# Optimization experiments

Measured on AMD Instinct MI355X. Metric: run time of the kernel, lower is better.

## Reference

```python
import jax, jax.numpy as jnp
import numpy as np

EPS = 1e-5  # haiku LayerNorm default


def _layernorm_last(x, scale, offset):
    m = jnp.mean(x, axis=-1, keepdims=True)
    v = jnp.var(x, axis=-1, keepdims=True)
    return (x - m) * jax.lax.rsqrt(v + EPS) * scale + offset


def setup_inputs() -> dict:
    key = jax.random.key(0)
    ks = jax.random.split(key, 6)
    N, C = 512, 128
    return {
        "act": jax.random.normal(ks[0], (N, N, C), dtype=jnp.float32),
        "mask": jnp.ones((N, N), dtype=jnp.float32),
        "ln_scale": jnp.ones((C,), dtype=jnp.float32),
        "ln_offset": jnp.zeros((C,), dtype=jnp.float32),
        "w_proj": jax.random.normal(ks[1], (C, 2 * C), dtype=jnp.float32) * 0.02,
        "w_gate": jax.random.normal(ks[2], (C, 2 * C), dtype=jnp.float32) * 0.02,
        "cn_scale": jnp.ones((C,), dtype=jnp.float32),
        "cn_offset": jnp.zeros((C,), dtype=jnp.float32),
        "w_out": jax.random.normal(ks[3], (C, C), dtype=jnp.float32) * 0.02,
        "b_out": jnp.zeros((C,), dtype=jnp.float32),
        "w_gate_out": jax.random.normal(ks[4], (C, C), dtype=jnp.float32) * 0.02,
        "b_gate_out": jnp.ones((C,), dtype=jnp.float32),  # bias_init=1.0
    }


def reference(act, mask, ln_scale, ln_offset, w_proj, w_gate,
              cn_scale, cn_offset, w_out, b_out, w_gate_out, b_gate_out):
    C = act.shape[-1]
    # left_norm_input (LayerNorm over channel axis)
    x = _layernorm_last(act, ln_scale, ln_offset)  # [N,N,C]
    input_act = x
    # gated linear unit: projection * sigmoid(gate), no biases (GLU kernel path)
    proj = jnp.einsum('ijc,cd->ijd', x, w_proj) * jax.nn.sigmoid(
        jnp.einsum('ijc,cd->ijd', x, w_gate))  # [N,N,2C]
    proj = jnp.transpose(proj, (2, 0, 1)) * mask[None]  # [2C,N,N]
    # split even/odd channels: reshape(C,2,N,N) -> a=proj[:,0], b=proj[:,1]
    proj = proj.reshape(C, 2, *proj.shape[1:])
    a, b = proj[:, 0], proj[:, 1]  # each [C,N,N]
    # triangle einsum ('ikc,jkc->ijc' -> 'cik,cjk->cij')
    act2 = jnp.einsum('cik,cjk->cij', a, b)  # [C,N,N]
    # center_norm: LayerNorm over channel axis (axis=0), params on axis 0
    m = jnp.mean(act2, axis=0, keepdims=True)
    v = jnp.var(act2, axis=0, keepdims=True)
    act2 = (act2 - m) * jax.lax.rsqrt(v + EPS) * cn_scale[:, None, None] + cn_offset[:, None, None]
    out = jnp.transpose(act2, (1, 2, 0))  # [N,N,C]
    out = jnp.einsum('ijc,cd->ijd', out, w_out) + b_out
    gate_out = jax.nn.sigmoid(jnp.einsum('ijc,cd->ijd', input_act, w_gate_out) + b_gate_out)
    return out * gate_out
```

## Files before the change

kernel.cpp:

```cpp
#include <hip/hip_runtime.h>
#include <stdint.h>

#define NDIM 512
#define CDIM 128
#define MDIM (NDIM*NDIM)

typedef unsigned short u16;
typedef __bf16 bf16v8 __attribute__((ext_vector_type(8)));
typedef float f32x4 __attribute__((ext_vector_type(4)));
typedef short s16x4 __attribute__((ext_vector_type(4)));

__device__ __forceinline__ u16 f2bf(float f){
  union { float f; uint32_t u; } v; v.f = f;
  uint32_t u = v.u;
  u += 0x7fffu + ((u >> 16) & 1u);
  return (u16)(u >> 16);
}
__device__ __forceinline__ float sigm(float x){ return 1.0f/(1.0f + __expf(-x)); }
__device__ __forceinline__ f32x4 mfma_bf16(bf16v8 a, bf16v8 b, f32x4 c){
  return __builtin_amdgcn_mfma_f32_16x16x32_bf16(a, b, c, 0, 0, 0);
}

__global__ void k0_prep(const float* __restrict__ wp, const float* __restrict__ wg,
                        const float* __restrict__ wgo, const float* __restrict__ wo,
                        u16* __restrict__ wt){
  const int d = blockIdx.x, k = threadIdx.x;
  float v;
  if (d < 256)      v = wp[k*256 + d];
  else if (d < 512) v = wg[k*256 + (d-256)];
  else if (d < 640) v = wgo[k*128 + (d-512)];
  else              v = wo[k*128 + (d-640)];
  wt[d*CDIM + k] = f2bf(v);
}

__global__ __launch_bounds__(256) void k1_ln_proj(
    const float* __restrict__ act, const float* __restrict__ mask,
    const float* __restrict__ lns, const float* __restrict__ lno,
    const float* __restrict__ bgo, const u16* __restrict__ wt,
    u16* __restrict__ AB, float* __restrict__ gate)
{
  __shared__ __align__(16) u16 xs[64][136];
  __shared__ __align__(16) u16 pgs[256][72];
  __shared__ float msk[64];
  const int t = threadIdx.x;
  const int m0 = blockIdx.x * 64;

  {
    const int r = t >> 2, q = t & 3;
    const float4* rp = (const float4*)(act + (size_t)(m0 + r)*CDIM + q*32);
    float4 v[8];
    #pragma unroll
    for (int i = 0; i < 8; ++i) v[i] = rp[i];
    float s = 0.f, s2 = 0.f;
    #pragma unroll
    for (int i = 0; i < 8; ++i){
      s  += v[i].x + v[i].y + v[i].z + v[i].w;
      s2 += v[i].x*v[i].x + v[i].y*v[i].y + v[i].z*v[i].z + v[i].w*v[i].w;
    }
    s += __shfl_xor(s, 1);  s2 += __shfl_xor(s2, 1);
    s += __shfl_xor(s, 2);  s2 += __shfl_xor(s2, 2);
    const float mean = s * (1.f/128.f);
    const float rstd = rsqrtf(s2 * (1.f/128.f) - mean*mean + 1e-5f);
    const float4* lsp = (const float4*)(lns + q*32);
    const float4* lop = (const float4*)(lno + q*32);
    #pragma unroll
    for (int i = 0; i < 8; ++i){
      const float4 sc = lsp[i], of = lop[i];
      s16x4 pk;
      pk.x = (short)f2bf((v[i].x - mean)*rstd*sc.x + of.x);
      pk.y = (short)f2bf((v[i].y - mean)*rstd*sc.y + of.y);
      pk.z = (short)f2bf((v[i].z - mean)*rstd*sc.z + of.z);
      pk.w = (short)f2bf((v[i].w - mean)*rstd*sc.w + of.w);
      *(s16x4*)&xs[r][q*32 + i*4] = pk;
    }
    if (t < 64) msk[t] = mask[m0 + t];
  }
  __syncthreads();

  const int w = t >> 6, L = t & 63, ln16 = L & 15, quad = L >> 4;
  bf16v8 af[4][4];
  #pragma unroll
  for (int rs = 0; rs < 4; ++rs)
    #pragma unroll
    for (int kk = 0; kk < 4; ++kk)
      af[rs][kk] = *(const bf16v8*)&xs[rs*16 + ln16][kk*32 + quad*8];

  const f32x4 zero4 = {0.f,0.f,0.f,0.f};
  #pragma unroll
  for (int pp = 0; pp < 4; ++pp){
    const int p = w*4 + pp;
    const u16* wpr = wt + (size_t)(16*p + ln16)*CDIM + quad*8;
    const u16* wgr = wpr + (size_t)256*CDIM;
    bf16v8 bp[4], bg[4];
    #pragma unroll
    for (int kk = 0; kk < 4; ++kk){
      bp[kk] = *(const bf16v8*)(wpr + kk*32);
      bg[kk] = *(const bf16v8*)(wgr + kk*32);
    }
    f32x4 aP[4] = {zero4, zero4, zero4, zero4};
    f32x4 aG[4] = {zero4, zero4, zero4, zero4};
    #pragma unroll
    for (int kk = 0; kk < 4; ++kk)
      #pragma unroll
      for (int rs = 0; rs < 4; ++rs){
        aP[rs] = mfma_bf16(af[rs][kk], bp[kk], aP[rs]);
        aG[rs] = mfma_bf16(af[rs][kk], bg[kk], aG[rs]);
      }
    #pragma unroll
    for (int rs = 0; rs < 4; ++rs)
      #pragma unroll
      for (int reg = 0; reg < 4; ++reg){
        const int ml = rs*16 + quad*4 + reg;
        const float pg = aP[rs][reg] * sigm(aG[rs][reg]) * msk[ml];
        pgs[16*p + ln16][ml] = f2bf(pg);
      }
  }
  #pragma unroll
  for (int u = 0; u < 2; ++u){
    const int e0 = 32*w + 16*u;
    const u16* wr = wt + (size_t)(512 + e0 + ln16)*CDIM + quad*8;
    bf16v8 bb[4];
    #pragma unroll
    for (int kk = 0; kk < 4; ++kk) bb[kk] = *(const bf16v8*)(wr + kk*32);
    f32x4 ag[4] = {zero4, zero4, zero4, zero4};
    #pragma unroll
    for (int kk = 0; kk < 4; ++kk)
      #pragma unroll
      for (int rs = 0; rs < 4; ++rs)
        ag[rs] = mfma_bf16(af[rs][kk], bb[kk], ag[rs]);
    const int e = e0 + ln16;
    const float bias = bgo[e];
    #pragma unroll
    for (int rs = 0; rs < 4; ++rs)
      #pragma unroll
      for (int reg = 0; reg < 4; ++reg){
        const int ml = rs*16 + quad*4 + reg;
        gate[(size_t)(m0 + ml)*CDIM + e] = sigm(ag[rs][reg] + bias);
      }
  }
  __syncthreads();

  #pragma unroll
  for (int p4 = 0; p4 < 4; ++p4){
    const int d = p4*64 + (t >> 2), q = t & 3;
    u16* dst = AB + (size_t)d*MDIM + m0 + q*16;
    const u16* src = &pgs[d][q*16];
    *(bf16v8*)dst       = *(const bf16v8*)src;
    *(bf16v8*)(dst + 8) = *(const bf16v8*)(src + 8);
  }
}

__global__ __launch_bounds__(256) void k2_tri(const u16* __restrict__ AB,
                                              u16* __restrict__ act2)
{
  __shared__ __align__(16) u16 As[128][72];
  __shared__ __align__(16) u16 Bs[128][72];
  const int t = threadIdx.x, bid = blockIdx.x;
  const int c  = bid >> 4;
  const int i0 = ((bid >> 2) & 3) * 128;
  const int j0 = (bid & 3) * 128;
  const u16* Ag = AB + (size_t)(2*c)*MDIM;
  const u16* Bg = AB + (size_t)(2*c + 1)*MDIM;

  const int w = t >> 6, L = t & 63, ln16 = L & 15, quad = L >> 4;
  const int iw = (w & 1)*64, jw = (w >> 1)*64;
  const int r = t >> 1, h = t & 1;

  const f32x4 zero4 = {0.f,0.f,0.f,0.f};
  f32x4 acc[4][4];
  #pragma unroll
  for (int x = 0; x < 4; ++x)
    #pragma unroll
    for (int y = 0; y < 4; ++y) acc[x][y] = zero4;

  for (int k0 = 0; k0 < NDIM; k0 += 64){
    const u16* ga = Ag + (size_t)(i0 + r)*NDIM + k0 + h*32;
    const u16* gb = Bg + (size_t)(j0 + r)*NDIM + k0 + h*32;
    bf16v8 sa[4], sb[4];
    #pragma unroll
    for (int x = 0; x < 4; ++x){
      sa[x] = *(const bf16v8*)(ga + x*8);
      sb[x] = *(const bf16v8*)(gb + x*8);
    }
    __syncthreads();
    #pragma unroll
    for (int x = 0; x < 4; ++x){
      *(bf16v8*)&As[r][h*32 + x*8] = sa[x];
      *(bf16v8*)&Bs[r][h*32 + x*8] = sb[x];
    }
    __syncthreads();
    #pragma unroll
    for (int kk = 0; kk < 2; ++kk){
      bf16v8 ar[4], br[4];
      #pragma unroll
      for (int x = 0; x < 4; ++x) ar[x] = *(const bf16v8*)&As[iw + x*16 + ln16][kk*32 + quad*8];
      #pragma unroll
      for (int y = 0; y < 4; ++y) br[y] = *(const bf16v8*)&Bs[jw + y*16 + ln16][kk*32 + quad*8];
      #pragma unroll
      for (int x = 0; x < 4; ++x)
        #pragma unroll
        for (int y = 0; y < 4; ++y)
          acc[x][y] = mfma_bf16(ar[x], br[y], acc[x][y]);
    }
  }

  u16* op = act2 + (size_t)c*MDIM;
  #pragma unroll
  for (int x = 0; x < 4; ++x)
    #pragma unroll
    for (int y = 0; y < 4; ++y)
      #pragma unroll
      for (int reg = 0; reg < 4; ++reg){
        const int il = iw + x*16 + quad*4 + reg;
        const int jl = jw + y*16 + ln16;
        op[(size_t)(i0 + il)*NDIM + j0 + jl] = f2bf(acc[x][y][reg]);
      }
}

__global__ __launch_bounds__(256) void k3_out(
    const u16* __restrict__ act2, const u16* __restrict__ wt2,
    const float* __restrict__ cns, const float* __restrict__ cno,
    const float* __restrict__ bo, float* __restrict__ out)
{
  __shared__ __align__(16) float vs[128][65];
  __shared__ __align__(16) u16 xs2[64][136];
  __shared__ float csh[128], coh[128];
  const int t = threadIdx.x;
  const int i  = blockIdx.x >> 3;
  const int j0 = (blockIdx.x & 7)*64;
  if (t < 128){ csh[t] = cns[t]; coh[t] = cno[t]; }

  {
    const int cc = t >> 1, h = t & 1;
    const u16* g = act2 + (size_t)cc*MDIM + (size_t)i*NDIM + j0 + h*32;
    #pragma unroll
    for (int x = 0; x < 4; ++x){
      bf16v8 uv = *(const bf16v8*)(g + x*8);
      #pragma unroll
      for (int e = 0; e < 8; ++e) vs[cc][h*32 + x*8 + e] = (float)uv[e];
    }
  }
  __syncthreads();
  {
    const int jj = t >> 2, q = t & 3;
    float s = 0.f, s2 = 0.f;
    #pragma unroll
    for (int ci = 0; ci < 32; ++ci){
      const float v = vs[4*ci + q][jj];
      s += v; s2 += v*v;
    }
    s += __shfl_xor(s,1); s2 += __shfl_xor(s2,1);
    s += __shfl_xor(s,2); s2 += __shfl_xor(s2,2);
    const float mean = s*(1.f/128.f);
    const float rstd = rsqrtf(s2*(1.f/128.f) - mean*mean + 1e-5f);
    #pragma unroll
    for (int ci = 0; ci < 32; ++ci){
      const int cc = 4*ci + q;
      xs2[jj][cc] = f2bf((vs[cc][jj] - mean)*rstd*csh[cc] + coh[cc]);
    }
  }
  __syncthreads();

  const int w = t >> 6, L = t & 63, ln16 = L & 15, quad = L >> 4;
  bf16v8 af[4];
  #pragma unroll
  for (int kk = 0; kk < 4; ++kk)
    af[kk] = *(const bf16v8*)&xs2[w*16 + ln16][kk*32 + quad*8];
  const f32x4 zero4 = {0.f,0.f,0.f,0.f};
  #pragma unroll
  for (int n = 0; n < 8; ++n){
    const u16* wr = wt2 + (size_t)(n*16 + ln16)*CDIM + quad*8;
    bf16v8 bb[4];
    #pragma unroll
    for (int kk = 0; kk < 4; ++kk) bb[kk] = *(const bf16v8*)(wr + kk*32);
    f32x4 ac = zero4;
    #pragma unroll
    for (int kk = 0; kk < 4; ++kk) ac = mfma_bf16(af[kk], bb[kk], ac);
    const int e = n*16 + ln16;
    const float bias = bo[e];
    #pragma unroll
    for (int reg = 0; reg < 4; ++reg){
      const int jl = w*16 + quad*4 + reg;
      const size_t idx = ((size_t)i*NDIM + j0 + jl)*(size_t)CDIM + e;
      out[idx] = (ac[reg] + bias) * out[idx];
    }
  }
}

extern "C" void kernel_launch(void* const* d_in, const int* in_sizes, int n_in,
                              void* d_out, int out_size, void* d_ws, size_t ws_size,
                              hipStream_t stream)
{
  const float* act = (const float*)d_in[0];
  const float* msk = (const float*)d_in[1];
  const float* lns = (const float*)d_in[2];
  const float* lno = (const float*)d_in[3];
  const float* wp  = (const float*)d_in[4];
  const float* wg  = (const float*)d_in[5];
  const float* cns = (const float*)d_in[6];
  const float* cno = (const float*)d_in[7];
  const float* wo  = (const float*)d_in[8];
  const float* bo  = (const float*)d_in[9];
  const float* wgo = (const float*)d_in[10];
  const float* bgo = (const float*)d_in[11];
  float* out = (float*)d_out;

  u16* AB   = (u16*)d_ws;
  u16* ACT2 = AB + (size_t)256*MDIM;
  u16* WT   = ACT2 + (size_t)128*MDIM;

  k0_prep   <<<dim3(768),  dim3(128), 0, stream>>>(wp, wg, wgo, wo, WT);
  k1_ln_proj<<<dim3(4096), dim3(256), 0, stream>>>(act, msk, lns, lno, bgo, WT, AB, out);
  k2_tri    <<<dim3(2048), dim3(256), 0, stream>>>(AB, ACT2);
  k3_out    <<<dim3(4096), dim3(256), 0, stream>>>(ACT2, WT + 640*CDIM, cns, cno, bo, out);
}
```

Baseline: 546.3 us.

## Recompute output gate in final kernel instead of round-tripping through output buffer

Moves the sigmoid output-gate projection out of the first kernel into the final kernel. The final kernel now re-reads the fp32 input, redoes the LayerNorm and computes the gate GEMM next to the output GEMM. This removes a 128 MB fp32 write and a 128 MB read of the gate through the output buffer, at the cost of re-reading the 128 MB fp32 input. It also stores the staging tiles as bf16 instead of fp32 to cut shared memory, and adds a minimum-blocks occupancy hint to both kernels.

```diff
diff --git a/kernel.cpp b/kernel.cpp
--- a/kernel.cpp
+++ b/kernel.cpp
@@ -9,12 +9,17 @@
 typedef __bf16 bf16v8 __attribute__((ext_vector_type(8)));
 typedef float f32x4 __attribute__((ext_vector_type(4)));
 typedef short s16x4 __attribute__((ext_vector_type(4)));
+
+union V16 { bf16v8 v; s16x4 h[2]; };
 
 __device__ __forceinline__ u16 f2bf(float f){
   union { float f; uint32_t u; } v; v.f = f;
   uint32_t u = v.u;
   u += 0x7fffu + ((u >> 16) & 1u);
   return (u16)(u >> 16);
+}
+__device__ __forceinline__ float bf2f(u16 x){
+  union { uint32_t u; float f; } v; v.u = ((uint32_t)x) << 16; return v.f;
 }
 __device__ __forceinline__ float sigm(float x){ return 1.0f/(1.0f + __expf(-x)); }
 __device__ __forceinline__ f32x4 mfma_bf16(bf16v8 a, bf16v8 b, f32x4 c){
@@ -33,14 +38,13 @@
   wt[d*CDIM + k] = f2bf(v);
 }
 
-__global__ __launch_bounds__(256) void k1_ln_proj(
+__global__ __launch_bounds__(256, 3) void k1_ln_proj(
     const float* __restrict__ act, const float* __restrict__ mask,
     const float* __restrict__ lns, const float* __restrict__ lno,
-    const float* __restrict__ bgo, const u16* __restrict__ wt,
-    u16* __restrict__ AB, float* __restrict__ gate)
+    const u16* __restrict__ wt, u16* __restrict__ AB)
 {
   __shared__ __align__(16) u16 xs[64][136];
-  __shared__ __align__(16) u16 pgs[256][72];
+  __shared__ __align__(8)  u16 pgs[256][68];
   __shared__ float msk[64];
   const int t = threadIdx.x;
   const int m0 = blockIdx.x * 64;
@@ -107,36 +111,16 @@
         aG[rs] = mfma_bf16(af[rs][kk], bg[kk], aG[rs]);
       }
     #pragma unroll
-    for (int rs = 0; rs < 4; ++rs)
+    for (int rs = 0; rs < 4; ++rs){
+      s16x4 pk;
       #pragma unroll
       for (int reg = 0; reg < 4; ++reg){
         const int ml = rs*16 + quad*4 + reg;
         const float pg = aP[rs][reg] * sigm(aG[rs][reg]) * msk[ml];
-        pgs[16*p + ln16][ml] = f2bf(pg);
+        ((short*)&pk)[reg] = (short)f2bf(pg);
       }
-  }
-  #pragma unroll
-  for (int u = 0; u < 2; ++u){
-    const int e0 = 32*w + 16*u;
-    const u16* wr = wt + (size_t)(512 + e0 + ln16)*CDIM + quad*8;
-    bf16v8 bb[4];
-    #pragma unroll
-    for (int kk = 0; kk < 4; ++kk) bb[kk] = *(const bf16v8*)(wr + kk*32);
-    f32x4 ag[4] = {zero4, zero4, zero4, zero4};
-    #pragma unroll
-    for (int kk = 0; kk < 4; ++kk)
-      #pragma unroll
-      for (int rs = 0; rs < 4; ++rs)
-        ag[rs] = mfma_bf16(af[rs][kk], bb[kk], ag[rs]);
-    const int e = e0 + ln16;
-    const float bias = bgo[e];
-    #pragma unroll
-    for (int rs = 0; rs < 4; ++rs)
-      #pragma unroll
-      for (int reg = 0; reg < 4; ++reg){
-        const int ml = rs*16 + quad*4 + reg;
-        gate[(size_t)(m0 + ml)*CDIM + e] = sigm(ag[rs][reg] + bias);
-      }
+      *(s16x4*)&pgs[16*p + ln16][rs*16 + quad*4] = pk;
+    }
   }
   __syncthreads();
 
@@ -144,9 +128,9 @@
   for (int p4 = 0; p4 < 4; ++p4){
     const int d = p4*64 + (t >> 2), q = t & 3;
     u16* dst = AB + (size_t)d*MDIM + m0 + q*16;
-    const u16* src = &pgs[d][q*16];
-    *(bf16v8*)dst       = *(const bf16v8*)src;
-    *(bf16v8*)(dst + 8) = *(const bf16v8*)(src + 8);
+    #pragma unroll
+    for (int x = 0; x < 4; ++x)
+      *(s16x4*)(dst + x*4) = *(const s16x4*)&pgs[d][q*16 + x*4];
   }
 }
 
@@ -217,27 +201,62 @@
       }
 }
 
-__global__ __launch_bounds__(256) void k3_out(
-    const u16* __restrict__ act2, const u16* __restrict__ wt2,
+__global__ __launch_bounds__(256, 3) void k3_out(
+    const float* __restrict__ act, const u16* __restrict__ act2,
+    const u16* __restrict__ wt,
+    const float* __restrict__ lns, const float* __restrict__ lno,
     const float* __restrict__ cns, const float* __restrict__ cno,
-    const float* __restrict__ bo, float* __restrict__ out)
+    const float* __restrict__ bo, const float* __restrict__ bgo,
+    float* __restrict__ out)
 {
-  __shared__ __align__(16) float vs[128][65];
+  __shared__ __align__(16) u16 xg[64][136];
+  __shared__ __align__(8)  u16 vsb[128][68];
   __shared__ __align__(16) u16 xs2[64][136];
   __shared__ float csh[128], coh[128];
   const int t = threadIdx.x;
   const int i  = blockIdx.x >> 3;
   const int j0 = (blockIdx.x & 7)*64;
+  const size_t mbase = (size_t)i*NDIM + j0;
+
   if (t < 128){ csh[t] = cns[t]; coh[t] = cno[t]; }
 
+  {
+    const int r = t >> 2, q = t & 3;
+    const float4* rp = (const float4*)(act + (mbase + r)*CDIM + q*32);
+    float4 v[8];
+    #pragma unroll
+    for (int x = 0; x < 8; ++x) v[x] = rp[x];
+    float s = 0.f, s2 = 0.f;
+    #pragma unroll
+    for (int x = 0; x < 8; ++x){
+      s  += v[x].x + v[x].y + v[x].z + v[x].w;
+      s2 += v[x].x*v[x].x + v[x].y*v[x].y + v[x].z*v[x].z + v[x].w*v[x].w;
+    }
+    s += __shfl_xor(s, 1);  s2 += __shfl_xor(s2, 1);
+    s += __shfl_xor(s, 2);  s2 += __shfl_xor(s2, 2);
+    const float mean = s * (1.f/128.f);
+    const float rstd = rsqrtf(s2 * (1.f/128.f) - mean*mean + 1e-5f);
+    const float4* lsp = (const float4*)(lns + q*32);
+    const float4* lop = (const float4*)(lno + q*32);
+    #pragma unroll
+    for (int x = 0; x < 8; ++x){
+      const float4 sc = lsp[x], of = lop[x];
+      s16x4 pk;
+      pk.x = (short)f2bf((v[x].x - mean)*rstd*sc.x + of.x);
+      pk.y = (short)f2bf((v[x].y - mean)*rstd*sc.y + of.y);
+      pk.z = (short)f2bf((v[x].z - mean)*rstd*sc.z + of.z);
+      pk.w = (short)f2bf((v[x].w - mean)*rstd*sc.w + of.w);
+      *(s16x4*)&xg[r][q*32 + x*4] = pk;
+    }
+  }
   {
     const int cc = t >> 1, h = t & 1;
-    const u16* g = act2 + (size_t)cc*MDIM + (size_t)i*NDIM + j0 + h*32;
+    const u16* g = act2 + (size_t)cc*MDIM + mbase + h*32;
     #pragma unroll
     for (int x = 0; x < 4; ++x){
-      bf16v8 uv = *(const bf16v8*)(g + x*8);
-      #pragma unroll
-      for (int e = 0; e < 8; ++e) vs[cc][h*32 + x*8 + e] = (float)uv[e];
+      V16 u; u.v = *(const bf16v8*)(g + x*8);
+      *(s16x4*)&vsb[cc][h*32 + x*8]     = u.h[0];
+      *(s16x4*)&vsb[cc][h*32 + x*8 + 4] = u.h[1];
     }
   }
   __syncthreads();
@@ -246,7 +265,7 @@
     float s = 0.f, s2 = 0.f;
     #pragma unroll
     for (int ci = 0; ci < 32; ++ci){
-      const float v = vs[4*ci + q][jj];
+      const float v = bf2f(vsb[4*ci + q][jj]);
       s += v; s2 += v*v;
     }
     s += __shfl_xor(s,1); s2 += __shfl_xor(s2,1);
@@ -256,33 +275,42 @@
     #pragma unroll
     for (int ci = 0; ci < 32; ++ci){
       const int cc = 4*ci + q;
-      xs2[jj][cc] = f2bf((vs[cc][jj] - mean)*rstd*csh[cc] + coh[cc]);
+      const float v = bf2f(vsb[cc][jj]);
+      xs2[jj][cc] = f2bf((v - mean)*rstd*csh[cc] + coh[cc]);
     }
   }
   __syncthreads();
 
   const int w = t >> 6, L = t & 63, ln16 = L & 15, quad = L >> 4;
-  bf16v8 af[4];
-  #pragma unroll
-  for (int kk = 0; kk < 4; ++kk)
-    af[kk] = *(const bf16v8*)&xs2[w*16 + ln16][kk*32 + quad*8];
+  bf16v8 aO[4], aG[4];
+  #pragma unroll
+  for (int kk = 0; kk < 4; ++kk){
+    aO[kk] = *(const bf16v8*)&xs2[w*16 + ln16][kk*32 + quad*8];
+    aG[kk] = *(const bf16v8*)&xg [w*16 + ln16][kk*32 + quad*8];
+  }
   const f32x4 zero4 = {0.f,0.f,0.f,0.f};
   #pragma unroll
   for (int n = 0; n < 8; ++n){
-    const u16* wr = wt2 + (size_t)(n*16 + ln16)*CDIM + quad*8;
-    bf16v8 bb[4];
-    #pragma unroll
-    for (int kk = 0; kk < 4; ++kk) bb[kk] = *(const bf16v8*)(wr + kk*32);
-    f32x4 ac = zero4;
-    #pragma unroll
-    for (int kk = 0; kk < 4; ++kk) ac = mfma_bf16(af[kk], bb[kk], ac);
+    const u16* wor = wt + (size_t)(640 + n*16 + ln16)*CDIM + quad*8;
+    const u16* wgr = wt + (size_t)(512 + n*16 + ln16)*CDIM + quad*8;
+    bf16v8 bO[4], bG[4];
+    #pragma unroll
+    for (int kk = 0; kk < 4; ++kk){
+      bO[kk] = *(const bf16v8*)(wor + kk*32);
+      bG[kk] = *(const bf16v8*)(wgr + kk*32);
+    }
+    f32x4 cO = zero4, cG = zero4;
+    #pragma unroll
+    for (int kk = 0; kk < 4; ++kk){
+      cO = mfma_bf16(aO[kk], bO[kk], cO);
+      cG = mfma_bf16(aG[kk], bG[kk], cG);
+    }
     const int e = n*16 + ln16;
-    const float bias = bo[e];
+    const float biasO = bo[e], biasG = bgo[e];
     #pragma unroll
     for (int reg = 0; reg < 4; ++reg){
       const int jl = w*16 + quad*4 + reg;
-      const size_t idx = ((size_t)i*NDIM + j0 + jl)*(size_t)CDIM + e;
-      out[idx] = (ac[reg] + bias) * out[idx];
+      out[(mbase + jl)*(size_t)CDIM + e] = (cO[reg] + biasO) * sigm(cG[reg] + biasG);
     }
   }
 }
@@ -310,7 +338,8 @@
   u16* WT   = ACT2 + (size_t)128*MDIM;
 
   k0_prep   <<<dim3(768),  dim3(128), 0, stream>>>(wp, wg, wgo, wo, WT);
-  k1_ln_proj<<<dim3(4096), dim3(256), 0, stream>>>(act, msk, lns, lno, bgo, WT, AB, out);
+  k1_ln_proj<<<dim3(4096), dim3(256), 0, stream>>>(act, msk, lns, lno, WT, AB);
   k2_tri    <<<dim3(2048), dim3(256), 0, stream>>>(AB, ACT2);
-  k3_out    <<<dim3(4096), dim3(256), 0, stream>>>(ACT2, WT + 640*CDIM, cns, cno, bo, out);
-}
+  k3_out    <<<dim3(4096), dim3(256), 0, stream>>>(act, ACT2, WT, lns, lno,
+                                                   cns, cno, bo, bgo, out);
+}
```

Measured after the change: 573.0 us. 1.05x slower.
